# Optimization experiments

Measured on AMD Instinct MI355X. Metric: run time of the kernel, lower is better.

## Reference

```python
import jax, jax.numpy as jnp
import numpy as np

BANDLIMIT = 0.5
STEP_SCALE = 1.0  # refiner default step_scale_value
LN_EPS = 1e-5


def _layernorm(x, g, b):
    mu = jnp.mean(x, axis=-1, keepdims=True)
    xc = x - mu
    inv = jax.lax.rsqrt(jnp.mean(xc * xc, axis=-1, keepdims=True) + LN_EPS)
    return xc * inv * g + b


def setup_inputs() -> dict:
    key = jax.random.key(0)
    ks = jax.random.split(key, 12)
    B, C, H, W = 16, 384, 64, 64
    P = 192  # conj-sym half of state_dim=384
    x = jax.random.normal(ks[0], (B, C, H, W), dtype=jnp.float32)
    ln1_g = 1.0 + 0.1 * jax.random.normal(ks[1], (C,), dtype=jnp.float32)
    ln1_b = 0.1 * jax.random.normal(ks[2], (C,), dtype=jnp.float32)
    # stable diagonal A: negative real part, HiPPO-like imaginary ladder
    lam_re = -(0.3 + jax.random.uniform(ks[3], (P,), dtype=jnp.float32))
    lam_im = jnp.pi * jnp.arange(P, dtype=jnp.float32)
    Lambda = jnp.stack([lam_re, lam_im], axis=-1)          # [P,2] (re,im)
    Bmat = jax.random.normal(ks[4], (P, C, 2), dtype=jnp.float32) / np.sqrt(C)
    Cmat = jax.random.normal(ks[5], (C, P, 2), dtype=jnp.float32) / np.sqrt(P)
    D = jax.random.normal(ks[6], (C,), dtype=jnp.float32)
    log_step = jax.random.uniform(ks[7], (P,), dtype=jnp.float32,
                                  minval=float(np.log(1e-3)), maxval=float(np.log(0.1)))
    ln2_g = 1.0 + 0.1 * jax.random.normal(ks[8], (C,), dtype=jnp.float32)
    ln2_b = 0.1 * jax.random.normal(ks[9], (C,), dtype=jnp.float32)
    W_enc = jax.random.normal(ks[10], (2 * C, C), dtype=jnp.float32) / np.sqrt(C)
    W_dec = jax.random.normal(ks[11], (C, C), dtype=jnp.float32) / np.sqrt(C)
    return {"x": x, "ln1_g": ln1_g, "ln1_b": ln1_b, "Lambda": Lambda,
            "Bmat": Bmat, "Cmat": Cmat, "D": D, "log_step": log_step,
            "ln2_g": ln2_g, "ln2_b": ln2_b, "W_enc": W_enc, "W_dec": W_dec}


def reference(x, ln1_g, ln1_b, Lambda, Bmat, Cmat, D, log_step, ln2_g, ln2_b, W_enc, W_dec):
    Bsz, C, H, W = x.shape
    u = x.reshape(Bsz, C, H * W).transpose(0, 2, 1)        # [B, L, C]

    # --- S5Block: attn branch ---
    fx = _layernorm(u, ln1_g, ln1_b)
    res = fx

    lam = Lambda[..., 0] + 1j * Lambda[..., 1]             # [P] complex
    Bc = Bmat[..., 0] + 1j * Bmat[..., 1]                  # [P, C]
    Cc = Cmat[..., 0] + 1j * Cmat[..., 1]                  # [C, P]
    step = STEP_SCALE * jnp.exp(log_step)                  # [P]
    # bandlimit mask on C (as in S5 with bandlimit=0.5)
    freqs = (step / STEP_SCALE) * jnp.abs(Lambda[..., 1]) / (2.0 * jnp.pi)
    mask = (freqs < BANDLIMIT * 0.5).astype(Cc.dtype)
    Cc = Cc * mask
    # ZOH discretization
    lam_bar = jnp.exp(lam * step)                          # [P]
    B_bar = ((lam_bar - 1.0) / lam)[:, None] * Bc          # [P, C]
    Bu = jnp.einsum('ph,blh->blp', B_bar, fx.astype(B_bar.dtype))  # [B,L,P] complex
    lam_el = jnp.broadcast_to(lam_bar, Bu.shape)

    def binop(a, b):
        # linear recurrence composition: x <- a2*(a1*x + b1) + b2
        return a[0] * b[0], b[0] * a[1] + b[1]

    _, xs = jax.lax.associative_scan(binop, (lam_el, Bu), axis=1)  # [B,L,P]
    y = 2.0 * jnp.real(jnp.einsum('hp,blp->blh', Cc, xs)) + D * fx
    y = jax.nn.gelu(y, approximate=False) + res

    # --- S5Block: GEGLU FFN branch ---
    fy = _layernorm(y, ln2_g, ln2_b)
    z = fy @ W_enc.T                                       # [B,L,2C]
    z1, z2 = jnp.split(z, 2, axis=-1)
    z = z1 * jax.nn.gelu(z2, approximate=False)
    y = z @ W_dec.T + fy

    return y.transpose(0, 2, 1).reshape(Bsz, C, H, W)
```

## Files before the change

kernel.cpp:

```cpp
#include <hip/hip_runtime.h>
#include <hip/hip_bf16.h>
#include <math.h>

typedef __attribute__((ext_vector_type(4))) float f32x4;
typedef __attribute__((ext_vector_type(8))) short s16x8;
typedef unsigned short u16;
typedef unsigned int u32;

#define CDIM 384
#define PDIM 192
#define LDIM 4096
#define BSZ  16
#define MDIM 65536
#define KD   384
#define BM 128
#define BN 128
#define BK 32

__device__ __forceinline__ u16 f2bf(float f) {
    u32 x = __float_as_uint(f);
    x += 0x7fffu + ((x >> 16) & 1u);
    return (u16)(x >> 16);
}
__device__ __forceinline__ float bf2f(u16 v) {
    return __uint_as_float(((u32)v) << 16);
}
__device__ __forceinline__ float gelu_exact(float x) {
    return 0.5f * x * (1.0f + erff(x * 0.7071067811865476f));
}
__device__ __forceinline__ float gelu_fast(float x) {
    float w = -1.5957691216f * x * (1.0f + 0.044715f * x * x);
    return x / (1.0f + __expf(w));
}
__device__ __forceinline__ void gld_lds16(const u16* g, u16* l) {
    __builtin_amdgcn_global_load_lds(
        (const __attribute__((address_space(1))) void*)g,
        (__attribute__((address_space(3))) void*)l, 16, 0, 0);
}

__global__ __launch_bounds__(256) void k_setup(
    const float* __restrict__ Lambda, const float* __restrict__ Bmat,
    const float* __restrict__ Cmat, const float* __restrict__ log_step,
    const float* __restrict__ W_enc, const float* __restrict__ W_dec,
    u16* __restrict__ Wb, u16* __restrict__ Wc, u16* __restrict__ We,
    u16* __restrict__ Wd, float* __restrict__ lam_bar)
{
    int idx = blockIdx.x * 256 + threadIdx.x;
    if (idx < 73728) {
        int p = idx / CDIM, c = idx % CDIM;
        float st  = expf(log_step[p]);
        float lre = Lambda[2*p], lim = Lambda[2*p+1];
        float el  = expf(lre * st);
        float lbr = el * cosf(lim * st);
        float lbi = el * sinf(lim * st);
        float dd  = lre*lre + lim*lim;
        float a = lbr - 1.0f, b = lbi;
        float cr = (a * lre + b * lim) / dd;
        float ci = (b * lre - a * lim) / dd;
        float Br = Bmat[2*(p*CDIM + c)], Bi = Bmat[2*(p*CDIM + c) + 1];
        Wb[p*KD + c]          = f2bf(cr*Br - ci*Bi);
        Wb[(PDIM + p)*KD + c] = f2bf(cr*Bi + ci*Br);
    } else if (idx < 147456) {
        int e = idx - 73728;
        int h = e / PDIM, p = e % PDIM;
        float st  = expf(log_step[p]);
        float lim = Lambda[2*p+1];
        float freq = st * fabsf(lim) / 6.283185307179586f;
        float sc = (freq < 0.25f) ? 2.0f : 0.0f;
        Wc[h*KD + p]        = f2bf( sc * Cmat[2*(h*PDIM + p)]);
        Wc[h*KD + PDIM + p] = f2bf(-sc * Cmat[2*(h*PDIM + p) + 1]);
    } else if (idx < 442368) {
        int e = idx - 147456;
        We[e] = f2bf(W_enc[e]);
    } else if (idx < 589824) {
        int e = idx - 442368;
        Wd[e] = f2bf(W_dec[e]);
    } else if (idx < 590016) {
        int p = idx - 589824;
        float st  = expf(log_step[p]);
        float lre = Lambda[2*p], lim = Lambda[2*p+1];
        float el  = expf(lre * st);
        lam_bar[2*p]   = el * cosf(lim * st);
        lam_bar[2*p+1] = el * sinf(lim * st);
    }
}

__global__ __launch_bounds__(256) void k_ln1(
    const float* __restrict__ x, const float* __restrict__ g,
    const float* __restrict__ bb, u16* __restrict__ fx)
{
    __shared__ float tile[CDIM * 36];
    __shared__ float mu_sh[32], inv_sh[32];
    int b  = blockIdx.x >> 7;
    int l0 = (blockIdx.x & 127) * 32;
    int tid = threadIdx.x;
    const float* src = x + ((size_t)b * CDIM) * LDIM + l0;
    #pragma unroll
    for (int it = 0; it < 12; it++) {
        int s = it * 256 + tid;
        int ch = s >> 3, c4 = (s & 7) * 4;
        float4 v = *(const float4*)(src + (size_t)ch * LDIM + c4);
        *(float4*)(tile + ch * 36 + c4) = v;
    }
    __syncthreads();
    int j = tid >> 3, k = tid & 7;
    float sum = 0.f, sq = 0.f;
    for (int c = k; c < CDIM; c += 8) {
        float v = tile[c * 36 + j];
        sum += v; sq += v * v;
    }
    sum += __shfl_xor(sum, 1); sq += __shfl_xor(sq, 1);
    sum += __shfl_xor(sum, 2); sq += __shfl_xor(sq, 2);
    sum += __shfl_xor(sum, 4); sq += __shfl_xor(sq, 4);
    float mu  = sum * (1.0f / CDIM);
    float var = sq * (1.0f / CDIM) - mu * mu;
    float inv = rsqrtf(var + 1e-5f);
    if (k == 0) { mu_sh[j] = mu; inv_sh[j] = inv; }
    __syncthreads();
    u16* dst = fx + ((size_t)(b * LDIM + l0)) * CDIM;
    #pragma unroll
    for (int it = 0; it < 12; it++) {
        int s  = it * 256 + tid;
        int cq = s % 96, jj = s / 96;
        int c  = cq * 4;
        float m2 = mu_sh[jj], iv = inv_sh[jj];
        float4 gv = *(const float4*)(g + c);
        float4 bv = *(const float4*)(bb + c);
        ushort4 o;
        o.x = f2bf((tile[(c+0)*36 + jj] - m2) * iv * gv.x + bv.x);
        o.y = f2bf((tile[(c+1)*36 + jj] - m2) * iv * gv.y + bv.y);
        o.z = f2bf((tile[(c+2)*36 + jj] - m2) * iv * gv.z + bv.z);
        o.w = f2bf((tile[(c+3)*36 + jj] - m2) * iv * gv.w + bv.w);
        *(ushort4*)(dst + (size_t)jj * CDIM + c) = o;
    }
}

template<bool SWAP>
__device__ __forceinline__ void gemm_core(
    const u16* __restrict__ A, int lda, const u16* __restrict__ Bw,
    int m0, int n0, u16* a_sh, u16* b_sh, f32x4 acc[4][4])
{
    const int tid  = threadIdx.x;
    const int w    = tid >> 6, lane = tid & 63;
    const int t16  = lane & 15, quad = lane >> 4;
    const int wm   = w >> 1,   wn   = w & 1;
    const int lr  = lane >> 2;
    const int cbg = (lane & 3) ^ ((lane >> 3) & 3);
    const u16* gA0 = A  + (size_t)(m0 + w*32 + lr) * lda + cbg*8;
    const u16* gA1 = gA0 + (size_t)16 * lda;
    const u16* gB0 = Bw + (size_t)(n0 + w*32 + lr) * KD + cbg*8;
    const u16* gB1 = gB0 + (size_t)16 * KD;
    u16* lA0 = a_sh + (w*32) * BK;
    u16* lA1 = lA0 + 16*BK;
    u16* lB0 = b_sh + (w*32) * BK;
    u16* lB1 = lB0 + 16*BK;
    const int pos = (quad ^ ((t16 >> 1) & 3)) * 8;
    const u16* ard = a_sh + (wm*64 + t16) * BK + pos;
    const u16* brd = b_sh + (wn*64 + t16) * BK + pos;
    #pragma unroll
    for (int i = 0; i < 4; i++)
        #pragma unroll
        for (int j = 0; j < 4; j++) acc[i][j] = (f32x4){0.f,0.f,0.f,0.f};
    for (int kb = 0; kb < KD; kb += BK) {
        __syncthreads();
        gld_lds16(gA0 + kb, lA0);
        gld_lds16(gA1 + kb, lA1);
        gld_lds16(gB0 + kb, lB0);
        gld_lds16(gB1 + kb, lB1);
        __syncthreads();
        s16x8 af[4], bfr[4];
        #pragma unroll
        for (int i = 0; i < 4; i++) af[i]  = *(const s16x8*)(ard + i*16*BK);
        #pragma unroll
        for (int j = 0; j < 4; j++) bfr[j] = *(const s16x8*)(brd + j*16*BK);
        #pragma unroll
        for (int i = 0; i < 4; i++)
            #pragma unroll
            for (int j = 0; j < 4; j++) {
                if (SWAP)
                    acc[i][j] = __builtin_amdgcn_mfma_f32_16x16x32_bf16(bfr[j], af[i], acc[i][j], 0,0,0);
                else
                    acc[i][j] = __builtin_amdgcn_mfma_f32_16x16x32_bf16(af[i], bfr[j], acc[i][j], 0,0,0);
            }
    }
}

__global__ __launch_bounds__(256) void k_gemm_bu(
    const u16* __restrict__ fx, const u16* __restrict__ Wb, u16* __restrict__ Bu)
{
    __shared__ __align__(16) u16 a_sh[BM*BK], b_sh[BN*BK];
    int m0 = blockIdx.x * BM, n0 = blockIdx.y * BN;
    f32x4 acc[4][4];
    gemm_core<false>(fx, CDIM, Wb, m0, n0, a_sh, b_sh, acc);
    int lane = threadIdx.x & 63, w = threadIdx.x >> 6;
    int t16 = lane & 15, quad = lane >> 4, wm = w >> 1, wn = w & 1;
    #pragma unroll
    for (int i = 0; i < 4; i++)
        #pragma unroll
        for (int j = 0; j < 4; j++)
            #pragma unroll
            for (int rr = 0; rr < 4; rr++) {
                int m = m0 + wm*64 + i*16 + quad*4 + rr;
                int n = n0 + wn*64 + j*16 + t16;
                Bu[(size_t)m * CDIM + n] = f2bf(acc[i][j][rr]);
            }
}

__global__ __launch_bounds__(256) void k_gemm_y(
    const u16* __restrict__ xs, const u16* __restrict__ Wc,
    const u16* __restrict__ fx, const float* __restrict__ Dv, u16* __restrict__ y)
{
    __shared__ __align__(16) u16 a_sh[BM*BK], b_sh[BN*BK];
    int m0 = blockIdx.x * BM, n0 = blockIdx.y * BN;
    f32x4 acc[4][4];
    gemm_core<false>(xs, CDIM, Wc, m0, n0, a_sh, b_sh, acc);
    int lane = threadIdx.x & 63, w = threadIdx.x >> 6;
    int t16 = lane & 15, quad = lane >> 4, wm = w >> 1, wn = w & 1;
    float dv[4];
    #pragma unroll
    for (int j = 0; j < 4; j++) dv[j] = Dv[n0 + wn*64 + j*16 + t16];
    #pragma unroll
    for (int i = 0; i < 4; i++)
        #pragma unroll
        for (int j = 0; j < 4; j++)
            #pragma unroll
            for (int rr = 0; rr < 4; rr++) {
                int m = m0 + wm*64 + i*16 + quad*4 + rr;
                int n = n0 + wn*64 + j*16 + t16;
                float fxv = bf2f(fx[(size_t)m * CDIM + n]);
                float v = acc[i][j][rr] + dv[j] * fxv;
                y[(size_t)m * CDIM + n] = f2bf(gelu_fast(v) + fxv);
            }
}

__global__ __launch_bounds__(256) void k_gemm_zg(
    const u16* __restrict__ fy, const u16* __restrict__ We, u16* __restrict__ zg)
{
    __shared__ __align__(16) u16 sh[8448];
    u16* a_sh = sh;
    u16* b_sh = sh + BM*BK;
    const int tid = threadIdx.x;
    const int w = tid >> 6, lane = tid & 63;
    const int t16 = lane & 15, quad = lane >> 4;
    const int wm = w >> 1, wn = w & 1;
    const int m0 = blockIdx.x * BM;
    const int c0 = blockIdx.y * 64;
    const int lr  = lane >> 2;
    const int cbg = (lane & 3) ^ ((lane >> 3) & 3);
    const u16* gA0 = fy + (size_t)(m0 + w*32 + lr) * CDIM + cbg*8;
    const u16* gA1 = gA0 + (size_t)16 * CDIM;
    int brow = c0 + w*32 + ((w >= 2) ? 320 : 0);
    const u16* gB0 = We + (size_t)(brow + lr) * KD + cbg*8;
    const u16* gB1 = gB0 + (size_t)16 * KD;
    u16* lA0 = a_sh + (w*32) * BK;
    u16* lA1 = lA0 + 16*BK;
    u16* lB0 = b_sh + (w*32) * BK;
    u16* lB1 = lB0 + 16*BK;
    const int pos = (quad ^ ((t16 >> 1) & 3)) * 8;
    const u16* ard = a_sh + (wm*64 + t16) * BK + pos;
    const u16* brd = b_sh + (wn*64 + t16) * BK + pos;
    f32x4 acc[4][4];
    #pragma unroll
    for (int i = 0; i < 4; i++)
        #pragma unroll
        for (int j = 0; j < 4; j++) acc[i][j] = (f32x4){0.f,0.f,0.f,0.f};
    for (int kb = 0; kb < KD; kb += BK) {
        __syncthreads();
        gld_lds16(gA0 + kb, lA0);
        gld_lds16(gA1 + kb, lA1);
        gld_lds16(gB0 + kb, lB0);
        gld_lds16(gB1 + kb, lB1);
        __syncthreads();
        s16x8 af[4], bfr[4];
        #pragma unroll
        for (int i = 0; i < 4; i++) af[i]  = *(const s16x8*)(ard + i*16*BK);
        #pragma unroll
        for (int j = 0; j < 4; j++) bfr[j] = *(const s16x8*)(brd + j*16*BK);
        #pragma unroll
        for (int i = 0; i < 4; i++)
            #pragma unroll
            for (int j = 0; j < 4; j++)
                acc[i][j] = __builtin_amdgcn_mfma_f32_16x16x32_bf16(af[i], bfr[j], acc[i][j], 0,0,0);
    }
    __syncthreads();
    if (wn == 1) {
        #pragma unroll
        for (int i = 0; i < 4; i++)
            #pragma unroll
            for (int j = 0; j < 4; j++)
                #pragma unroll
                for (int rr = 0; rr < 4; rr++) {
                    int m = wm*64 + i*16 + quad*4 + rr;
                    int c = j*16 + t16;
                    sh[m*66 + c] = f2bf(gelu_fast(acc[i][j][rr]));
                }
    }
    __syncthreads();
    if (wn == 0) {
        #pragma unroll
        for (int i = 0; i < 4; i++)
            #pragma unroll
            for (int j = 0; j < 4; j++)
                #pragma unroll
                for (int rr = 0; rr < 4; rr++) {
                    int m = wm*64 + i*16 + quad*4 + rr;
                    int c = j*16 + t16;
                    float gv = bf2f(sh[m*66 + c]);
                    zg[(size_t)(m0 + m) * CDIM + c0 + c] = f2bf(acc[i][j][rr] * gv);
                }
    }
}

__global__ __launch_bounds__(256) void k_gemm_out(
    const u16* __restrict__ zg, const u16* __restrict__ Wd,
    const u16* __restrict__ fy, float* __restrict__ out)
{
    __shared__ __align__(16) u16 a_sh[BM*BK], b_sh[BN*BK];
    int m0 = blockIdx.x * BM, n0 = blockIdx.y * BN;
    f32x4 acc[4][4];
    gemm_core<true>(zg, CDIM, Wd, m0, n0, a_sh, b_sh, acc);
    int lane = threadIdx.x & 63, w = threadIdx.x >> 6;
    int t16 = lane & 15, quad = lane >> 4, wm = w >> 1, wn = w & 1;
    int b = m0 >> 12;
    #pragma unroll
    for (int i = 0; i < 4; i++)
        #pragma unroll
        for (int j = 0; j < 4; j++)
            #pragma unroll
            for (int rr = 0; rr < 4; rr++) {
                int nn = n0 + wn*64 + j*16 + quad*4 + rr;
                int mm = m0 + wm*64 + i*16 + t16;
                float fyv = bf2f(fy[(size_t)mm * CDIM + nn]);
                int l = mm & 4095;
                out[((size_t)(b * CDIM + nn)) * LDIM + l] = acc[i][j][rr] + fyv;
            }
}

__global__ __launch_bounds__(192) void k_scan_a(
    const u16* __restrict__ Bu, const float* __restrict__ lam_bar,
    float* __restrict__ summ)
{
    int b = blockIdx.x >> 6, ch = blockIdx.x & 63;
    int p = threadIdx.x;
    float lr = lam_bar[2*p], li = lam_bar[2*p+1];
    float xr = 0.f, xi = 0.f;
    const u16* base = Bu + (size_t)(b * LDIM + ch * 64) * CDIM;
    #pragma unroll 8
    for (int i = 0; i < 64; i++) {
        float br = bf2f(base[(size_t)i * CDIM + p]);
        float bi = bf2f(base[(size_t)i * CDIM + PDIM + p]);
        float nr = lr * xr - li * xi + br;
        float ni = lr * xi + li * xr + bi;
        xr = nr; xi = ni;
    }
    size_t o = (size_t)(b * 64 + ch) * CDIM + p;
    summ[o] = xr;
    summ[o + PDIM] = xi;
}

__global__ __launch_bounds__(256) void k_scan_b(
    const float* __restrict__ lam_bar, float* __restrict__ summ)
{
    int id = blockIdx.x * 256 + threadIdx.x;
    if (id >= BSZ * PDIM) return;
    int b = id / PDIM, p = id % PDIM;
    float ar = lam_bar[2*p], ai = lam_bar[2*p+1];
    #pragma unroll
    for (int s = 0; s < 6; s++) {
        float nr = ar * ar - ai * ai, ni = 2.f * ar * ai;
        ar = nr; ai = ni;
    }
    float cr = 0.f, ci = 0.f;
    #pragma unroll 4
    for (int ch = 0; ch < 64; ch++) {
        size_t o = (size_t)(b * 64 + ch) * CDIM + p;
        float sr = summ[o], si = summ[o + PDIM];
        summ[o] = cr; summ[o + PDIM] = ci;
        float nr = ar * cr - ai * ci + sr;
        float ni = ar * ci + ai * cr + si;
        cr = nr; ci = ni;
    }
}

__global__ __launch_bounds__(192) void k_scan_c(
    u16* __restrict__ Bu, const float* __restrict__ lam_bar,
    const float* __restrict__ summ)
{
    int b = blockIdx.x >> 6, ch = blockIdx.x & 63;
    int p = threadIdx.x;
    float lr = lam_bar[2*p], li = lam_bar[2*p+1];
    size_t oc = (size_t)(b * 64 + ch) * CDIM + p;
    float xr = summ[oc], xi = summ[oc + PDIM];
    u16* base = Bu + (size_t)(b * LDIM + ch * 64) * CDIM;
    #pragma unroll 8
    for (int i = 0; i < 64; i++) {
        float br = bf2f(base[(size_t)i * CDIM + p]);
        float bi = bf2f(base[(size_t)i * CDIM + PDIM + p]);
        float nr = lr * xr - li * xi + br;
        float ni = lr * xi + li * xr + bi;
        xr = nr; xi = ni;
        base[(size_t)i * CDIM + p] = f2bf(xr);
        base[(size_t)i * CDIM + PDIM + p] = f2bf(xi);
    }
}

__global__ __launch_bounds__(256) void k_ln2(
    const u16* __restrict__ y, const float* __restrict__ g,
    const float* __restrict__ bb, u16* __restrict__ fy)
{
    int w = threadIdx.x >> 6, lane = threadIdx.x & 63;
    size_t m = (size_t)blockIdx.x * 4 + w;
    const u16* row = y + m * CDIM;
    float v[6];
    float sum = 0.f, sq = 0.f;
    #pragma unroll
    for (int i = 0; i < 6; i++) {
        v[i] = bf2f(row[lane + 64 * i]);
        sum += v[i]; sq += v[i] * v[i];
    }
    #pragma unroll
    for (int o = 1; o < 64; o <<= 1) {
        sum += __shfl_xor(sum, o); sq += __shfl_xor(sq, o);
    }
    float mu  = sum * (1.0f / CDIM);
    float var = sq * (1.0f / CDIM) - mu * mu;
    float inv = rsqrtf(var + 1e-5f);
    u16* dst = fy + m * CDIM;
    #pragma unroll
    for (int i = 0; i < 6; i++) {
        int c = lane + 64 * i;
        dst[c] = f2bf((v[i] - mu) * inv * g[c] + bb[c]);
    }
}

extern "C" void kernel_launch(void* const* d_in, const int* in_sizes, int n_in,
                              void* d_out, int out_size, void* d_ws, size_t ws_size,
                              hipStream_t stream)
{
    const float* x        = (const float*)d_in[0];
    const float* ln1_g    = (const float*)d_in[1];
    const float* ln1_b    = (const float*)d_in[2];
    const float* Lambda   = (const float*)d_in[3];
    const float* Bmat     = (const float*)d_in[4];
    const float* Cmat     = (const float*)d_in[5];
    const float* Dvec     = (const float*)d_in[6];
    const float* log_step = (const float*)d_in[7];
    const float* ln2_g    = (const float*)d_in[8];
    const float* ln2_b    = (const float*)d_in[9];
    const float* W_enc    = (const float*)d_in[10];
    const float* W_dec    = (const float*)d_in[11];

    char* ws = (char*)d_ws;
    const size_t HBF = (size_t)MDIM * CDIM * 2;
    u16* fx = (u16*)(ws);
    u16* fy = (u16*)(ws + HBF);
    u16* bu = (u16*)(ws + 2 * HBF);
    u16* zg = (u16*)(ws + 2 * HBF);
    char* wbase = ws + 3 * HBF;
    u16* Wb = (u16*)(wbase);
    u16* Wc = (u16*)(wbase + 294912);
    u16* We = (u16*)(wbase + 589824);
    u16* Wd = (u16*)(wbase + 1179648);
    float* lam_bar = (float*)(wbase + 1474560);
    float* summ    = (float*)(wbase + 1476096);
    u16* yb  = (u16*)d_out;
    float* out = (float*)d_out;

    k_setup<<<2305, 256, 0, stream>>>(Lambda, Bmat, Cmat, log_step, W_enc, W_dec,
                                      Wb, Wc, We, Wd, lam_bar);
    k_ln1<<<2048, 256, 0, stream>>>(x, ln1_g, ln1_b, fx);
    k_gemm_bu<<<dim3(512, 3), 256, 0, stream>>>(fx, Wb, bu);
    k_scan_a<<<1024, 192, 0, stream>>>(bu, lam_bar, summ);
    k_scan_b<<<12, 256, 0, stream>>>(lam_bar, summ);
    k_scan_c<<<1024, 192, 0, stream>>>(bu, lam_bar, summ);
    k_gemm_y<<<dim3(512, 3), 256, 0, stream>>>(bu, Wc, fx, Dvec, yb);
    k_ln2<<<16384, 256, 0, stream>>>(yb, ln2_g, ln2_b, fy);
    k_gemm_zg<<<dim3(512, 6), 256, 0, stream>>>(fy, We, zg);
    k_gemm_out<<<dim3(512, 3), 256, 0, stream>>>(zg, Wd, fy, out);
}
```

Baseline: 472.6 us.

## Compute paired GEGLU halves in-register and vectorize transposed output stores

The encoder GEMM now has each block compute both the value and gate halves (128 columns each) with two accumulator sets. The GEGLU product is then formed directly in registers, which removes the LDS round-trip and the idle half of the warps in the epilogue, and halves the grid. The output GEMM switches its gemm_core transpose mode so each thread holds four consecutive L positions and writes them as one float4 store into the channel-major output. The cost is doubled accumulator registers, which may lower occupancy.

```diff
diff --git a/kernel.cpp b/kernel.cpp
--- a/kernel.cpp
+++ b/kernel.cpp
@@ -236,79 +236,71 @@
 __global__ __launch_bounds__(256) void k_gemm_zg(
     const u16* __restrict__ fy, const u16* __restrict__ We, u16* __restrict__ zg)
 {
-    __shared__ __align__(16) u16 sh[8448];
-    u16* a_sh = sh;
-    u16* b_sh = sh + BM*BK;
+    __shared__ __align__(16) u16 a_sh[128*BK];
+    __shared__ __align__(16) u16 b_sh[256*BK];
     const int tid = threadIdx.x;
     const int w = tid >> 6, lane = tid & 63;
     const int t16 = lane & 15, quad = lane >> 4;
     const int wm = w >> 1, wn = w & 1;
     const int m0 = blockIdx.x * BM;
-    const int c0 = blockIdx.y * 64;
+    const int c0 = blockIdx.y * 128;
     const int lr  = lane >> 2;
     const int cbg = (lane & 3) ^ ((lane >> 3) & 3);
     const u16* gA0 = fy + (size_t)(m0 + w*32 + lr) * CDIM + cbg*8;
     const u16* gA1 = gA0 + (size_t)16 * CDIM;
-    int brow = c0 + w*32 + ((w >= 2) ? 320 : 0);
-    const u16* gB0 = We + (size_t)(brow + lr) * KD + cbg*8;
-    const u16* gB1 = gB0 + (size_t)16 * KD;
+    int browg = (w < 2) ? (c0 + w*64) : (384 + c0 + (w - 2)*64);
+    const u16* gB = We + (size_t)(browg + lr) * KD + cbg*8;
     u16* lA0 = a_sh + (w*32) * BK;
     u16* lA1 = lA0 + 16*BK;
-    u16* lB0 = b_sh + (w*32) * BK;
-    u16* lB1 = lB0 + 16*BK;
+    u16* lB  = b_sh + (w*64) * BK;
     const int pos = (quad ^ ((t16 >> 1) & 3)) * 8;
-    const u16* ard = a_sh + (wm*64 + t16) * BK + pos;
-    const u16* brd = b_sh + (wn*64 + t16) * BK + pos;
-    f32x4 acc[4][4];
-    #pragma unroll
-    for (int i = 0; i < 4; i++)
-        #pragma unroll
-        for (int j = 0; j < 4; j++) acc[i][j] = (f32x4){0.f,0.f,0.f,0.f};
+    const u16* ard  = a_sh + (wm*64 + t16) * BK + pos;
+    const u16* brd1 = b_sh + (wn*64 + t16) * BK + pos;
+    const u16* brd2 = brd1 + 128*BK;
+    f32x4 acc1[4][4], acc2[4][4];
+    #pragma unroll
+    for (int i = 0; i < 4; i++)
+        #pragma unroll
+        for (int j = 0; j < 4; j++) {
+            acc1[i][j] = (f32x4){0.f,0.f,0.f,0.f};
+            acc2[i][j] = (f32x4){0.f,0.f,0.f,0.f};
+        }
     for (int kb = 0; kb < KD; kb += BK) {
         __syncthreads();
         gld_lds16(gA0 + kb, lA0);
         gld_lds16(gA1 + kb, lA1);
-        gld_lds16(gB0 + kb, lB0);
-        gld_lds16(gB1 + kb, lB1);
+        gld_lds16(gB + kb,                    lB);
+        gld_lds16(gB + (size_t)16*KD + kb,    lB + 16*BK);
+        gld_lds16(gB + (size_t)32*KD + kb,    lB + 32*BK);
+        gld_lds16(gB + (size_t)48*KD + kb,    lB + 48*BK);
         __syncthreads();
-        s16x8 af[4], bfr[4];
-        #pragma unroll
-        for (int i = 0; i < 4; i++) af[i]  = *(const s16x8*)(ard + i*16*BK);
-        #pragma unroll
-        for (int j = 0; j < 4; j++) bfr[j] = *(const s16x8*)(brd + j*16*BK);
+        s16x8 af[4], b1[4], b2[4];
+        #pragma unroll
+        for (int i = 0; i < 4; i++) af[i] = *(const s16x8*)(ard + i*16*BK);
+        #pragma unroll
+        for (int j = 0; j < 4; j++) {
+            b1[j] = *(const s16x8*)(brd1 + j*16*BK);
+            b2[j] = *(const s16x8*)(brd2 + j*16*BK);
+        }
         #pragma unroll
         for (int i = 0; i < 4; i++)
             #pragma unroll
-            for (int j = 0; j < 4; j++)
-                acc[i][j] = __builtin_amdgcn_mfma_f32_16x16x32_bf16(af[i], bfr[j], acc[i][j], 0,0,0);
-    }
-    __syncthreads();
-    if (wn == 1) {
-        #pragma unroll
-        for (int i = 0; i < 4; i++)
-            #pragma unroll
-            for (int j = 0; j < 4; j++)
-                #pragma unroll
-                for (int rr = 0; rr < 4; rr++) {
-                    int m = wm*64 + i*16 + quad*4 + rr;
-                    int c = j*16 + t16;
-                    sh[m*66 + c] = f2bf(gelu_fast(acc[i][j][rr]));
-                }
-    }
-    __syncthreads();
-    if (wn == 0) {
-        #pragma unroll
-        for (int i = 0; i < 4; i++)
-            #pragma unroll
-            for (int j = 0; j < 4; j++)
-                #pragma unroll
-                for (int rr = 0; rr < 4; rr++) {
-                    int m = wm*64 + i*16 + quad*4 + rr;
-                    int c = j*16 + t16;
-                    float gv = bf2f(sh[m*66 + c]);
-                    zg[(size_t)(m0 + m) * CDIM + c0 + c] = f2bf(acc[i][j][rr] * gv);
-                }
-    }
+            for (int j = 0; j < 4; j++) {
+                acc1[i][j] = __builtin_amdgcn_mfma_f32_16x16x32_bf16(af[i], b1[j], acc1[i][j], 0,0,0);
+                acc2[i][j] = __builtin_amdgcn_mfma_f32_16x16x32_bf16(af[i], b2[j], acc2[i][j], 0,0,0);
+            }
+    }
+    #pragma unroll
+    for (int i = 0; i < 4; i++)
+        #pragma unroll
+        for (int j = 0; j < 4; j++)
+            #pragma unroll
+            for (int rr = 0; rr < 4; rr++) {
+                int m = m0 + wm*64 + i*16 + quad*4 + rr;
+                int c = c0 + wn*64 + j*16 + t16;
+                float gv = gelu_fast(acc2[i][j][rr]);
+                zg[(size_t)m * CDIM + c] = f2bf(acc1[i][j][rr] * gv);
+            }
 }
 
 __global__ __launch_bounds__(256) void k_gemm_out(
@@ -318,22 +310,23 @@
     __shared__ __align__(16) u16 a_sh[BM*BK], b_sh[BN*BK];
     int m0 = blockIdx.x * BM, n0 = blockIdx.y * BN;
     f32x4 acc[4][4];
-    gemm_core<true>(zg, CDIM, Wd, m0, n0, a_sh, b_sh, acc);
+    gemm_core<false>(zg, CDIM, Wd, m0, n0, a_sh, b_sh, acc);
     int lane = threadIdx.x & 63, w = threadIdx.x >> 6;
     int t16 = lane & 15, quad = lane >> 4, wm = w >> 1, wn = w & 1;
     int b = m0 >> 12;
     #pragma unroll
     for (int i = 0; i < 4; i++)
         #pragma unroll
-        for (int j = 0; j < 4; j++)
-            #pragma unroll
-            for (int rr = 0; rr < 4; rr++) {
-                int nn = n0 + wn*64 + j*16 + quad*4 + rr;
-                int mm = m0 + wm*64 + i*16 + t16;
-                float fyv = bf2f(fy[(size_t)mm * CDIM + nn]);
-                int l = mm & 4095;
-                out[((size_t)(b * CDIM + nn)) * LDIM + l] = acc[i][j][rr] + fyv;
-            }
+        for (int j = 0; j < 4; j++) {
+            int mm = m0 + wm*64 + i*16 + quad*4;
+            int nn = n0 + wn*64 + j*16 + t16;
+            f32x4 v = acc[i][j];
+            #pragma unroll
+            for (int rr = 0; rr < 4; rr++)
+                v[rr] += bf2f(fy[(size_t)(mm + rr) * CDIM + nn]);
+            int l = mm & 4095;
+            *(f32x4*)(out + ((size_t)(b * CDIM + nn)) * LDIM + l) = v;
+        }
 }
 
 __global__ __launch_bounds__(192) void k_scan_a(
@@ -475,6 +468,6 @@
     k_scan_c<<<1024, 192, 0, stream>>>(bu, lam_bar, summ);
     k_gemm_y<<<dim3(512, 3), 256, 0, stream>>>(bu, Wc, fx, Dvec, yb);
     k_ln2<<<16384, 256, 0, stream>>>(yb, ln2_g, ln2_b, fy);
-    k_gemm_zg<<<dim3(512, 6), 256, 0, stream>>>(fy, We, zg);
+    k_gemm_zg<<<dim3(512, 3), 256, 0, stream>>>(fy, We, zg);
     k_gemm_out<<<dim3(512, 3), 256, 0, stream>>>(zg, Wd, fy, out);
 }
```

Result: slower. 503.8 us (+6.6%).
